# Kernel tuning notes

Hardware: AMD Instinct MI355X
Metric: run time of the kernel (lower is better)

Reference implementation:

```python
import math
import jax, jax.numpy as jnp
import numpy as np

B, L, C = 64, 4096, 512
SPARSE_RATIO, AGGR_RATIO, DIM_RATIO = 0.5, 0.4, 0.2
K = math.ceil(L * SPARSE_RATIO)          # 2048 kept tokens
P = int(L * AGGR_RATIO * SPARSE_RATIO)   # 819 super tokens
H = int(C * DIM_RATIO)                   # 102 MLP hidden
LN_EPS = 1e-5


def setup_inputs() -> dict:
    key = jax.random.key(0)
    ks = jax.random.split(key, 6)
    return {
        "tokens": jax.random.normal(ks[0], (B, L, C), jnp.float32),
        "attention_x": jax.random.normal(ks[1], (B, L), jnp.float32),
        "attention_y": jax.random.normal(ks[2], (B, L), jnp.float32),
        "ln_g": jnp.ones((C,), jnp.float32),
        "ln_b": jnp.zeros((C,), jnp.float32),
        "w1": jax.random.normal(ks[3], (C, H), jnp.float32) * 0.02,
        "b1": jnp.zeros((H,), jnp.float32),
        "w2": jax.random.normal(ks[4], (H, P), jnp.float32) * 0.02,
        "b2": jnp.zeros((P,), jnp.float32),
        "scale": jnp.ones((1, 1, 1), jnp.float32),
    }


def reference(tokens, attention_x, attention_y, ln_g, ln_b, w1, b1, w2, b2, scale):
    # ---- TokenSparse ----
    score = attention_x + attention_y                      # [B, L]
    order = jnp.argsort(-score, axis=1)                    # descending sort indices
    score_sort = jnp.take_along_axis(score, order, axis=1)
    keep = order[:, :K]                                    # [B, K]
    score_mask = jnp.zeros_like(score).at[jnp.arange(B)[:, None], keep].set(1.0)
    select_tokens = jnp.take_along_axis(tokens, keep[:, :, None], axis=1)       # [B, K, C]
    non_tokens = jnp.take_along_axis(tokens, order[:, K:, None], axis=1)        # [B, L-K, C]
    non_w = jax.nn.softmax(score_sort[:, K:], axis=1)[..., None]                # [B, L-K, 1]
    extra_token = jnp.sum(non_tokens * non_w, axis=1, keepdims=True)            # [B, 1, C]
    all_tokens = jnp.concatenate([select_tokens, extra_token], axis=1)          # [B, K+1, C]

    # ---- TokenAggregation (keep_policy=None) ----
    mu = all_tokens.mean(-1, keepdims=True)
    var = all_tokens.var(-1, keepdims=True)
    xn = (all_tokens - mu) * jax.lax.rsqrt(var + LN_EPS) * ln_g + ln_b
    h = jax.nn.gelu(xn @ w1 + b1, approximate=False)       # [B, K+1, H]
    wgt = jnp.swapaxes(h @ w2 + b2, 1, 2) * scale          # [B, P, K+1]
    wgt = jax.nn.softmax(wgt, axis=2)
    super_tokens = jnp.einsum('bpk,bkc->bpc', wgt, all_tokens)  # [B, P, C]
    return super_tokens, score_mask
```

## Files before the change

### kernel.cpp

```cpp
#include <hip/hip_runtime.h>

typedef unsigned char u8;
typedef unsigned short u16;
typedef unsigned int u32;
typedef unsigned long long u64;
typedef __attribute__((ext_vector_type(8))) short short8;
typedef __attribute__((ext_vector_type(4))) float f32x4;

#define NB 64
#define LL 4096
#define CC 512
#define KK 2048
#define PPQ 819
#define HH 102
#define KP 2176
#define PPAD 896
#define HP 128
#define NCH 34
#define NRUN 33
#define NPT 13

__device__ __forceinline__ u16 f2bf(float f) {
  u32 u = __float_as_uint(f);
  u += 0x7fffu + ((u >> 16) & 1u);
  return (u16)(u >> 16);
}
__device__ __forceinline__ float bf2f(u16 h) { return __uint_as_float(((u32)h) << 16); }
__device__ __forceinline__ float dec_score(u32 s) {
  u32 u = (s & 0x80000000u) ? (s ^ 0x80000000u) : ~s;
  return __uint_as_float(u);
}
__device__ __forceinline__ u8 f2fp8(float f) {
  return (u8)(__builtin_amdgcn_cvt_pk_fp8_f32(f, 0.f, 0, false) & 0xff);
}

__global__ __launch_bounds__(1024) void sort_kernel(
    const float* __restrict__ ax, const float* __restrict__ ay,
    u64* __restrict__ keys, float* __restrict__ mask_out, float2* __restrict__ stats)
{
  __shared__ u64 arr[LL];
  __shared__ float red[16];
  int b = blockIdx.x, tid = threadIdx.x;
  for (int i = tid; i < LL; i += 1024) {
    float s = ax[(size_t)b*LL + i] + ay[(size_t)b*LL + i];
    u32 u = __float_as_uint(s);
    u = (u & 0x80000000u) ? ~u : (u | 0x80000000u);
    arr[i] = (((u64)u) << 32) | (u32)(LL - 1 - i);
  }
  __syncthreads();
  for (int k = 2; k <= LL; k <<= 1) {
    for (int j = k >> 1; j > 0; j >>= 1) {
      #pragma unroll
      for (int rep = 0; rep < 4; ++rep) {
        int i = tid + rep * 1024;
        int ixj = i ^ j;
        if (ixj > i) {
          u64 a = arr[i], c = arr[ixj];
          bool desc = ((i & k) == 0);
          if (desc ? (a < c) : (a > c)) { arr[i] = c; arr[ixj] = a; }
        }
      }
      __syncthreads();
    }
  }
  for (int i = tid; i < LL; i += 1024) {
    u64 v = arr[i];
    keys[(size_t)b*LL + i] = v;
    int idx = (LL - 1) - (int)(v & 0xffffffffu);
    mask_out[(size_t)b*LL + idx] = (i < KK) ? 1.0f : 0.0f;
  }
  float m = dec_score((u32)(arr[KK] >> 32));
  float part = 0.f;
  for (int i = KK + tid; i < LL; i += 1024)
    part += expf(dec_score((u32)(arr[i] >> 32)) - m);
  #pragma unroll
  for (int off = 32; off; off >>= 1) part += __shfl_xor(part, off);
  if ((tid & 63) == 0) red[tid >> 6] = part;
  __syncthreads();
  if (tid == 0) {
    float s = 0.f;
    #pragma unroll
    for (int i = 0; i < 16; ++i) s += red[i];
    stats[b] = make_float2(m, s);
  }
}

__global__ __launch_bounds__(256) void tail_partial_kernel(
    const float* __restrict__ tokens, const u64* __restrict__ keys,
    const float2* __restrict__ stats, float* __restrict__ partials)
{
  int b = blockIdx.y, rb = blockIdx.x, t = threadIdx.x;
  float m = stats[b].x, inv = 1.0f / stats[b].y;
  const u64* kb = keys + (size_t)b*LL + KK + rb*256;
  float a0 = 0.f, a1 = 0.f;
  #pragma unroll 4
  for (int r = 0; r < 256; ++r) {
    u64 kk = kb[r];
    int idx = (LL - 1) - (int)(kk & 0xffffffffu);
    float w = expf(dec_score((u32)(kk >> 32)) - m) * inv;
    const float* src = tokens + ((size_t)b*LL + idx)*CC;
    a0 += w * src[t];
    a1 += w * src[t + 256];
  }
  float* dst = partials + (size_t)(b*8 + rb)*CC;
  dst[t] = a0; dst[t + 256] = a1;
}

__global__ __launch_bounds__(512) void gather_ln_mlp_kernel(
    const float* __restrict__ tokens, const u64* __restrict__ keys,
    const float* __restrict__ partials,
    const u16* __restrict__ w1T,
    const float* __restrict__ b1,
    const float* __restrict__ ln_g, const float* __restrict__ ln_b,
    u8* __restrict__ allTT, u8* __restrict__ hbuf8)
{
  __shared__ u16 t[64*512];
  __shared__ float2 rst[64];
  int b = blockIdx.y;
  int r0 = blockIdx.x*64;
  int tid = threadIdx.x, lane = tid & 63, wave = tid >> 6;

  #pragma unroll
  for (int i = 0; i < 8; ++i) {
    int rr = wave*8 + i;
    int r = r0 + rr;
    float x[8];
    if (r < KK) {
      u64 kk = keys[(size_t)b*LL + r];
      int idx = (LL - 1) - (int)(kk & 0xffffffffu);
      const float* src = tokens + ((size_t)b*LL + idx)*CC + lane*8;
      f32x4 v0 = *(const f32x4*)src;
      f32x4 v1 = *(const f32x4*)(src + 4);
      #pragma unroll
      for (int j = 0; j < 4; ++j) { x[j] = v0[j]; x[j+4] = v1[j]; }
    } else if (r == KK) {
      #pragma unroll
      for (int j = 0; j < 8; ++j) {
        float s = 0.f;
        #pragma unroll
        for (int p = 0; p < 8; ++p) s += partials[(size_t)(b*8 + p)*CC + lane*8 + j];
        x[j] = s;
      }
    } else {
      #pragma unroll
      for (int j = 0; j < 8; ++j) x[j] = 0.f;
    }
    float s = 0.f;
    #pragma unroll
    for (int j = 0; j < 8; ++j) s += x[j];
    #pragma unroll
    for (int off = 32; off; off >>= 1) s += __shfl_xor(s, off);
    float mu = s * (1.0f/CC);
    float vs = 0.f;
    #pragma unroll
    for (int j = 0; j < 8; ++j) { float d = x[j] - mu; vs += d*d; }
    #pragma unroll
    for (int off = 32; off; off >>= 1) vs += __shfl_xor(vs, off);
    float rstd = rsqrtf(vs * (1.0f/CC) + 1e-5f);
    short8 raw;
    #pragma unroll
    for (int j = 0; j < 8; ++j) raw[j] = (short)f2bf(x[j]);
    *(short8*)(t + rr*512 + ((lane ^ (rr & 7)) << 3)) = raw;
    if (lane == 0) rst[rr] = make_float2(mu, rstd);
  }
  __syncthreads();

  {
    int c = tid;
    u8* dstg = allTT + ((size_t)(b*NCH + blockIdx.x))*(CC*64) + (size_t)(c >> 4)*1024;
    int ln16 = c & 15;
    int cu = c >> 3, cl = c & 7;
    float g = ln_g[c], bb = ln_b[c];
    #pragma unroll
    for (int g8 = 0; g8 < 8; ++g8) {
      float f[8];
      int ri[8];
      #pragma unroll
      for (int j = 0; j < 8; ++j) {
        int rr = g8*8 + j;
        ri[j] = rr*512 + (((cu ^ (rr & 7)) << 3) | cl);
        f[j] = bf2f(t[ri[j]]);
      }
      u32 lo = __builtin_amdgcn_cvt_pk_fp8_f32(f[0], f[1], 0, false);
      lo = __builtin_amdgcn_cvt_pk_fp8_f32(f[2], f[3], lo, true);
      u32 hi = __builtin_amdgcn_cvt_pk_fp8_f32(f[4], f[5], 0, false);
      hi = __builtin_amdgcn_cvt_pk_fp8_f32(f[6], f[7], hi, true);
      *(uint2*)(dstg + (g8 >> 2)*512 + (ln16 + (g8 & 3)*16)*8) = make_uint2(lo, hi);
      #pragma unroll
      for (int j = 0; j < 8; ++j) {
        int rr = g8*8 + j;
        float2 st = rst[rr];
        t[ri[j]] = f2bf((f[j] - st.x)*st.y*g + bb);
      }
    }
  }
  __syncthreads();

  {
    int colh = wave*16 + (lane & 15);
    f32x4 hacc[4];
    #pragma unroll
    for (int m = 0; m < 4; ++m) hacc[m] = (f32x4){0.f,0.f,0.f,0.f};
    for (int kt = 0; kt < 16; ++kt) {
      short8 bf = *(const short8*)(w1T + (size_t)colh*CC + kt*32 + (lane >> 4)*8);
      int ku = kt*4 + (lane >> 4);
      #pragma unroll
      for (int m = 0; m < 4; ++m) {
        int row = m*16 + (lane & 15);
        short8 afr = *(const short8*)(t + row*512 + ((ku ^ (row & 7)) << 3));
        hacc[m] = __builtin_amdgcn_mfma_f32_16x16x32_bf16(afr, bf, hacc[m], 0, 0, 0);
      }
    }
    float bb = (colh < HH) ? b1[colh] : 0.f;
    u8* hb = hbuf8 + (size_t)(b*NCH + blockIdx.x)*8192;
    int s4 = colh >> 5;
    int lq = (colh >> 3) & 3;
    int hbyte = colh & 7;
    #pragma unroll
    for (int m = 0; m < 4; ++m)
      #pragma unroll
      for (int q = 0; q < 4; ++q) {
        int rk = m*16 + (lane >> 4)*4 + q;
        float rv = 0.f;
        if (colh < HH) {
          float xx = hacc[m][q] + bb;
          rv = 0.5f*xx*(1.0f + erff(xx*0.70710678118654752f));
        }
        hb[(size_t)((rk >> 4)*4 + s4)*512 + ((rk & 15) + lq*16)*8 + hbyte] = f2fp8(4.0f*rv);
      }
  }
}

__global__ __launch_bounds__(256) void prep_kernel(
    const float* __restrict__ w1, const float* __restrict__ w2,
    u16* __restrict__ w1T, u8* __restrict__ w2T8)
{
  int id = blockIdx.x*256 + threadIdx.x;
  if (id < HP*CC) {
    int r = id >> 9, c = id & 511;
    w1T[id] = (r < HH) ? f2bf(w1[c*HH + r]) : (u16)0;
  } else {
    int id2 = id - HP*CC;
    if (id2 < PPAD*HP) {
      int r = id2 >> 7, c = id2 & 127;
      w2T8[id2] = (r < PPQ && c < HH) ? f2fp8(16.0f*w2[(size_t)c*PPQ + r]) : (u8)0;
    }
  }
}

template<bool MASKED>
__device__ __forceinline__ void v9_logits(
    const long (&af)[4], const u8* w2s, const float (&b2s2)[2],
    float sc2, int kcAbs, int kf, int pfb, int lane,
    float (&s_acc)[2], u8* psbuf)
{
  #pragma unroll
  for (int j = 0; j < 2; ++j) {
    int pr = (pfb + j)*16 + (lane & 15);
    long wf[4];
    #pragma unroll
    for (int s4 = 0; s4 < 4; ++s4)
      wf[s4] = *(const long*)(w2s + pr*128 + (((s4*4 + (lane >> 4)) ^ (pr & 14))*8));
    f32x4 Lacc = (f32x4){0.f,0.f,0.f,0.f};
    __builtin_amdgcn_s_setprio(1);
    #pragma unroll
    for (int s4 = 0; s4 < 4; ++s4)
      Lacc = __builtin_amdgcn_mfma_f32_16x16x32_fp8_fp8(af[s4], wf[s4], Lacc, 0, 0, 0);
    __builtin_amdgcn_s_setprio(0);
    float e[4];
    #pragma unroll
    for (int q = 0; q < 4; ++q) {
      e[q] = exp2f(fminf(fmaf(Lacc[q], sc2, b2s2[j]), 7.93482257f));
      if (MASKED) {
        int kg = kcAbs*64 + kf*16 + (lane >> 4)*4 + q;
        if (kg <= KK) s_acc[j] += e[q];
      } else {
        s_acc[j] += e[q];
      }
    }
    u32 w = __builtin_amdgcn_cvt_pk_fp8_f32(e[0], e[1], 0, false);
    w = __builtin_amdgcn_cvt_pk_fp8_f32(e[2], e[3], w, true);
    int kl = kf*16 + (lane >> 4)*4;
    *(u32*)(psbuf + pr*72 + kl) = w;
  }
}

__global__ __launch_bounds__(512, 4) void fused_kernel(
    const u8* __restrict__ hbuf8,
    const u8* __restrict__ w2T8,
    const u8* __restrict__ allTT,
    const float* __restrict__ b2, const float* __restrict__ scalep,
    float* __restrict__ out)
{
  __shared__ u8 w2s[64*128];
  __shared__ u8 ps[2][64*72];
  __shared__ float sums[64];

  int lg = (blockIdx.x & 7)*104 + (blockIdx.x >> 3);
  int b = lg / 13;
  int pt = lg - b*13;
  int p0 = pt*64;

  int tid = threadIdx.x, lane = tid & 63, wave = tid >> 6;
  int kf = wave & 3;
  int pfb = (wave >> 2)*2;
  int cw = wave*64;

  const u8* abt = allTT + (size_t)b*NCH*(CC*64);

  {
    int row = tid >> 3, u2 = (tid & 7)*2;
    uint4 v = *(const uint4*)(w2T8 + (size_t)(p0 + row)*HP + u2*8);
    *(uint4*)(w2s + row*128 + ((u2 ^ (row & 14))*8)) = v;
  }
  if (tid < 64) sums[tid] = 0.f;

  const u8* ab = hbuf8 + (size_t)b*NCH*8192 + (size_t)kf*2048 + lane*8;
  long af[4];
  #pragma unroll
  for (int s4 = 0; s4 < 4; ++s4) af[s4] = *(const long*)(ab + s4*512);

  float sclog = scalep[0] * 1.44269504f;
  float sc2 = sclog * (1.0f/64.0f);
  float b2s2[2];
  #pragma unroll
  for (int j = 0; j < 2; ++j) {
    int gp = p0 + (pfb + j)*16 + (lane & 15);
    b2s2[j] = ((gp < PPQ) ? b2[gp] : 0.f) * sclog;
  }

  float s_acc[2] = {0.f, 0.f};
  f32x4 acc[4][4];
  #pragma unroll
  for (int pf = 0; pf < 4; ++pf)
    #pragma unroll
    for (int cf = 0; cf < 4; ++cf) acc[pf][cf] = (f32x4){0.f,0.f,0.f,0.f};

  __syncthreads();

  for (int kc = 0; kc < NRUN; ++kc) {
    int pcur = kc & 1;

    if (kc < NRUN - 1)
      v9_logits<false>(af, w2s, b2s2, sc2, kc, kf, pfb, lane, s_acc, ps[pcur]);
    else
      v9_logits<true>(af, w2s, b2s2, sc2, kc, kf, pfb, lane, s_acc, ps[pcur]);

    if (kc + 1 < NRUN) {
      ab += 8192;
      #pragma unroll
      for (int s4 = 0; s4 < 4; ++s4) af[s4] = *(const long*)(ab + s4*512);
    }

    const u8* avb = abt + (size_t)kc*(CC*64);
    long bv0[4], bv1[4];
    #pragma unroll
    for (int cf = 0; cf < 4; ++cf) {
      const u8* cb = avb + (size_t)(wave*4 + cf)*1024 + lane*8;
      bv0[cf] = *(const long*)(cb);
      bv1[cf] = *(const long*)(cb + 512);
    }

    asm volatile("s_waitcnt lgkmcnt(0)" ::: "memory");
    __builtin_amdgcn_sched_barrier(0);
    __builtin_amdgcn_s_barrier();
    __builtin_amdgcn_sched_barrier(0);

    #pragma unroll
    for (int sl = 0; sl < 2; ++sl) {
      int koff = sl*32 + (lane >> 4)*8;
      long pa[4];
      #pragma unroll
      for (int pf = 0; pf < 4; ++pf)
        pa[pf] = *(const long*)(ps[pcur] + (pf*16 + (lane & 15))*72 + koff);
      __builtin_amdgcn_s_setprio(1);
      #pragma unroll
      for (int cf = 0; cf < 4; ++cf) {
        long bv = sl ? bv1[cf] : bv0[cf];
        #pragma unroll
        for (int pf = 0; pf < 4; ++pf)
          acc[pf][cf] = __builtin_amdgcn_mfma_f32_16x16x32_fp8_fp8(pa[pf], bv, acc[pf][cf], 0, 0, 0);
      }
      __builtin_amdgcn_s_setprio(0);
    }
  }

  #pragma unroll
  for (int j = 0; j < 2; ++j) {
    float s = s_acc[j];
    s += __shfl_xor(s, 16);
    s += __shfl_xor(s, 32);
    if (lane < 16) atomicAdd(&sums[(pfb + j)*16 + lane], s);
  }
  __syncthreads();

  #pragma unroll
  for (int pf = 0; pf < 4; ++pf)
    #pragma unroll
    for (int q = 0; q < 4; ++q) {
      int pl = pf*16 + (lane >> 4)*4 + q;
      int gp = p0 + pl;
      if (gp < PPQ) {
        float inv = 1.0f / sums[pl];
        #pragma unroll
        for (int cf = 0; cf < 4; ++cf) {
          int c = cw + cf*16 + (lane & 15);
          out[(size_t)b*PPQ*CC + (size_t)gp*CC + c] = acc[pf][cf][q]*inv;
        }
      }
    }
}

extern "C" void kernel_launch(void* const* d_in, const int* in_sizes, int n_in,
                              void* d_out, int out_size, void* d_ws, size_t ws_size,
                              hipStream_t stream)
{
  const float* tokens = (const float*)d_in[0];
  const float* ax  = (const float*)d_in[1];
  const float* ay  = (const float*)d_in[2];
  const float* ln_g = (const float*)d_in[3];
  const float* ln_b = (const float*)d_in[4];
  const float* w1  = (const float*)d_in[5];
  const float* b1  = (const float*)d_in[6];
  const float* w2  = (const float*)d_in[7];
  const float* b2  = (const float*)d_in[8];
  const float* scale = (const float*)d_in[9];
  float* out_super = (float*)d_out;
  float* out_mask  = out_super + (size_t)NB*PPQ*CC;

  char* ws = (char*)d_ws;
  size_t off = 0;
  u64* keys = (u64*)(ws + off);           off += (size_t)NB*LL*8;
  float2* stats = (float2*)(ws + off);    off += 512;
  float* partials = (float*)(ws + off);   off += (size_t)NB*8*CC*4;
  u8*  allTT = (u8*)(ws + off);           off += (size_t)NB*NCH*CC*64;
  u8*  hbuf8 = (u8*)(ws + off);           off += (size_t)NB*NCH*8192;
  u16* w1T   = (u16*)(ws + off);          off += (size_t)HP*CC*2;
  u8*  w2T8  = (u8*)(ws + off);           off += (size_t)PPAD*HP;
  if (off > ws_size) return;

  prep_kernel<<<704, 256, 0, stream>>>(w1, w2, w1T, w2T8);
  sort_kernel<<<NB, 1024, 0, stream>>>(ax, ay, keys, out_mask, stats);
  tail_partial_kernel<<<dim3(8, NB), 256, 0, stream>>>(tokens, keys, stats, partials);
  gather_ln_mlp_kernel<<<dim3(KP/64, NB), 512, 0, stream>>>(
      tokens, keys, partials, w1T, b1, ln_g, ln_b, allTT, hbuf8);
  fused_kernel<<<NB*NPT, 512, 0, stream>>>(
      hbuf8, w2T8, allTT, b2, scale, out_super);
}
```

Baseline: 403.3 us.

## Batch four K-chunks per barrier in fused softmax-PV loop

```diff
diff --git a/kernel.cpp b/kernel.cpp
--- a/kernel.cpp
+++ b/kernel.cpp
@@ -17,7 +17,6 @@
 #define PPAD 896
 #define HP 128
 #define NCH 34
-#define NRUN 33
 #define NPT 13
 
 __device__ __forceinline__ u16 f2bf(float f) {
@@ -285,6 +284,35 @@
   }
 }
 
+__device__ __forceinline__ void v9_pv(
+    const u8* psbuf, const u8* avb, int wave, int lane, f32x4 (&acc)[4][4])
+{
+  long bv0[4], bv1[4];
+  #pragma unroll
+  for (int cf = 0; cf < 4; ++cf) {
+    const u8* cb = avb + (size_t)(wave*4 + cf)*1024 + lane*8;
+    bv0[cf] = *(const long*)(cb);
+    bv1[cf] = *(const long*)(cb + 512);
+  }
+  #pragma unroll
+  for (int sl = 0; sl < 2; ++sl) {
+    int koff = sl*32 + (lane >> 4)*8;
+    long pa[4];
+    #pragma unroll
+    for (int pf = 0; pf < 4; ++pf)
+      pa[pf] = *(const long*)(psbuf + (pf*16 + (lane & 15))*72 + koff);
+    __builtin_amdgcn_s_setprio(1);
+    #pragma unroll
+    for (int cf = 0; cf < 4; ++cf) {
+      long bv = sl ? bv1[cf] : bv0[cf];
+      #pragma unroll
+      for (int pf = 0; pf < 4; ++pf)
+        acc[pf][cf] = __builtin_amdgcn_mfma_f32_16x16x32_fp8_fp8(pa[pf], bv, acc[pf][cf], 0, 0, 0);
+    }
+    __builtin_amdgcn_s_setprio(0);
+  }
+}
+
 __global__ __launch_bounds__(512, 4) void fused_kernel(
     const u8* __restrict__ hbuf8,
     const u8* __restrict__ w2T8,
@@ -293,7 +321,7 @@
     float* __restrict__ out)
 {
   __shared__ u8 w2s[64*128];
-  __shared__ u8 ps[2][64*72];
+  __shared__ u8 ps[4][64*72];
   __shared__ float sums[64];
 
   int lg = (blockIdx.x & 7)*104 + (blockIdx.x >> 3);
@@ -338,52 +366,35 @@
 
   __syncthreads();
 
-  for (int kc = 0; kc < NRUN; ++kc) {
-    int pcur = kc & 1;
-
-    if (kc < NRUN - 1)
-      v9_logits<false>(af, w2s, b2s2, sc2, kc, kf, pfb, lane, s_acc, ps[pcur]);
-    else
-      v9_logits<true>(af, w2s, b2s2, sc2, kc, kf, pfb, lane, s_acc, ps[pcur]);
-
-    if (kc + 1 < NRUN) {
+  for (int g = 0; g < 8; ++g) {
+    #pragma unroll
+    for (int u = 0; u < 4; ++u) {
+      int kc = g*4 + u;
+      v9_logits<false>(af, w2s, b2s2, sc2, kc, kf, pfb, lane, s_acc, ps[u]);
       ab += 8192;
       #pragma unroll
       for (int s4 = 0; s4 < 4; ++s4) af[s4] = *(const long*)(ab + s4*512);
     }
-
-    const u8* avb = abt + (size_t)kc*(CC*64);
-    long bv0[4], bv1[4];
-    #pragma unroll
-    for (int cf = 0; cf < 4; ++cf) {
-      const u8* cb = avb + (size_t)(wave*4 + cf)*1024 + lane*8;
-      bv0[cf] = *(const long*)(cb);
-      bv1[cf] = *(const long*)(cb + 512);
-    }
-
     asm volatile("s_waitcnt lgkmcnt(0)" ::: "memory");
     __builtin_amdgcn_sched_barrier(0);
     __builtin_amdgcn_s_barrier();
     __builtin_amdgcn_sched_barrier(0);
-
-    #pragma unroll
-    for (int sl = 0; sl < 2; ++sl) {
-      int koff = sl*32 + (lane >> 4)*8;
-      long pa[4];
-      #pragma unroll
-      for (int pf = 0; pf < 4; ++pf)
-        pa[pf] = *(const long*)(ps[pcur] + (pf*16 + (lane & 15))*72 + koff);
-      __builtin_amdgcn_s_setprio(1);
-      #pragma unroll
-      for (int cf = 0; cf < 4; ++cf) {
-        long bv = sl ? bv1[cf] : bv0[cf];
-        #pragma unroll
-        for (int pf = 0; pf < 4; ++pf)
-          acc[pf][cf] = __builtin_amdgcn_mfma_f32_16x16x32_fp8_fp8(pa[pf], bv, acc[pf][cf], 0, 0, 0);
-      }
-      __builtin_amdgcn_s_setprio(0);
-    }
-  }
+    #pragma unroll
+    for (int u = 0; u < 4; ++u) {
+      int kc = g*4 + u;
+      v9_pv(ps[u], abt + (size_t)kc*(CC*64), wave, lane, acc);
+    }
+    asm volatile("s_waitcnt lgkmcnt(0)" ::: "memory");
+    __builtin_amdgcn_sched_barrier(0);
+    __builtin_amdgcn_s_barrier();
+    __builtin_amdgcn_sched_barrier(0);
+  }
+  v9_logits<true>(af, w2s, b2s2, sc2, 32, kf, pfb, lane, s_acc, ps[0]);
+  asm volatile("s_waitcnt lgkmcnt(0)" ::: "memory");
+  __builtin_amdgcn_sched_barrier(0);
+  __builtin_amdgcn_s_barrier();
+  __builtin_amdgcn_sched_barrier(0);
+  v9_pv(ps[0], abt + (size_t)32*(CC*64), wave, lane, acc);
 
   #pragma unroll
   for (int j = 0; j < 2; ++j) {
```

After: 416.5 us. 1.03x slower.
